# Performance work log

Hardware: AMD Instinct MI355X
Metric: run time of the kernel (lower is better)

The kernel has to match this reference:

```python
import jax, jax.numpy as jnp
import numpy as np

D = 256; H = 8; HD = D // H; L = 6; NQ = 100; DFF = 2048
FREQS = np.geomspace(1.0, 512.0, 10).astype(np.float32)  # WorldSpacePE: 10 freqs up to 512


def _ln(x, g, b, eps=1e-5):
    m = x.mean(-1, keepdims=True)
    v = ((x - m) ** 2).mean(-1, keepdims=True)
    return (x - m) * jax.lax.rsqrt(v + eps) * g + b


def _mha(q, k, v, Wq, bq, Wk, bk, Wv, bv, Wo, bo, bias=None):
    # standard nn.MultiheadAttention math (batch_first, eval mode -> no dropout)
    B, Q, _ = q.shape; N = k.shape[1]
    qh = (q @ Wq + bq).reshape(B, Q, H, HD).transpose(0, 2, 1, 3)
    kh = (k @ Wk + bk).reshape(B, N, H, HD).transpose(0, 2, 1, 3)
    vh = (v @ Wv + bv).reshape(B, N, H, HD).transpose(0, 2, 1, 3)
    s = jnp.einsum('bhqd,bhkd->bhqk', qh, kh) / np.float32(np.sqrt(HD))
    if bias is not None:
        s = s + bias
    a = jax.nn.softmax(s, axis=-1)
    o = jnp.einsum('bhqk,bhkd->bhqd', a, vh).transpose(0, 2, 1, 3).reshape(B, Q, D)
    return o @ Wo + bo


def setup_inputs() -> dict:
    key = jax.random.key(0)
    cnt = [0]
    def nk():
        cnt[0] += 1
        return jax.random.fold_in(key, cnt[0])
    def rn(shape, scale=0.02):
        return (jax.random.normal(nk(), shape) * scale).astype(jnp.float32)
    def zeros(shape):
        return jnp.zeros(shape, jnp.float32)
    def ones(shape):
        return jnp.ones(shape, jnp.float32)
    B, N, NT = 8, 4096, 32
    inp = {
        'image_feats': jax.random.normal(nk(), (B, N, D), jnp.float32),
        'text_feats': jax.random.normal(nk(), (B, NT, 256), jnp.float32),
        'pointmap': jax.random.normal(nk(), (B, N, 3), jnp.float32),
        'query_embed': rn((NQ, D)),
        'presence_tok': rn((1, D)),
        'text_proj_W': rn((256, D)), 'text_proj_b': zeros((D,)),
        'tWq': rn((D, D)), 'tbq': zeros((D,)), 'tWk': rn((D, D)), 'tbk': zeros((D,)),
        'tWv': rn((D, D)), 'tbv': zeros((D,)), 'tWo': rn((D, D)), 'tbo': zeros((D,)),
        'tln_g': ones((D,)), 'tln_b': zeros((D,)),
        'wpe_W': rn((60, D)), 'wpe_b': zeros((D,)),
        'sa_Wq': rn((L, D, D)), 'sa_bq': zeros((L, D)), 'sa_Wk': rn((L, D, D)), 'sa_bk': zeros((L, D)),
        'sa_Wv': rn((L, D, D)), 'sa_bv': zeros((L, D)), 'sa_Wo': rn((L, D, D)), 'sa_bo': zeros((L, D)),
        'ca_Wq': rn((L, D, D)), 'ca_bq': zeros((L, D)), 'ca_Wk': rn((L, D, D)), 'ca_bk': zeros((L, D)),
        'ca_Wv': rn((L, D, D)), 'ca_bv': zeros((L, D)), 'ca_Wo': rn((L, D, D)), 'ca_bo': zeros((L, D)),
        'ffn_W1': rn((L, D, DFF)), 'ffn_b1': zeros((L, DFF)),
        'ffn_W2': rn((L, DFF, D)), 'ffn_b2': zeros((L, D)),
        'ln1_g': ones((L, D)), 'ln1_b': zeros((L, D)),
        'ln2_g': ones((L, D)), 'ln2_b': zeros((L, D)),
        'ln3_g': ones((L, D)), 'ln3_b': zeros((L, D)),
        'pos_W': rn((L, D, 3)), 'pos_b': zeros((L, 3)),
        'beta': ones((L, H)),  # gasa_beta_init = 1.0
        'fin_g': ones((D,)), 'fin_b': zeros((D,)),
        'pW1': rn((D, D)), 'pb1': zeros((D,)),
        'pW2': rn((D, D)), 'pb2': zeros((D,)),
        'pW3': rn((D, 1)), 'pb3': zeros((1,)),
    }
    return inp


def reference(image_feats, text_feats, pointmap, query_embed, presence_tok,
              text_proj_W, text_proj_b,
              tWq, tbq, tWk, tbk, tWv, tbv, tWo, tbo, tln_g, tln_b,
              wpe_W, wpe_b,
              sa_Wq, sa_bq, sa_Wk, sa_bk, sa_Wv, sa_bv, sa_Wo, sa_bo,
              ca_Wq, ca_bq, ca_Wk, ca_bk, ca_Wv, ca_bv, ca_Wo, ca_bo,
              ffn_W1, ffn_b1, ffn_W2, ffn_b2,
              ln1_g, ln1_b, ln2_g, ln2_b, ln3_g, ln3_b,
              pos_W, pos_b, beta, fin_g, fin_b,
              pW1, pb1, pW2, pb2, pW3, pb3):
    B, N, _ = image_feats.shape
    # --- world-space PE from pointmap (sin/cos over 10 freqs, 3 coords -> 60d -> D) ---
    ang = pointmap[..., None] * jnp.asarray(FREQS)            # [B,N,3,10]
    enc = jnp.concatenate([jnp.sin(ang), jnp.cos(ang)], -1).reshape(B, N, 60)
    mem = image_feats + enc @ wpe_W + wpe_b                   # PE added to memory
    # --- text conditioning of queries ---
    txt = text_feats @ text_proj_W + text_proj_b              # [B,NT,D]
    x = jnp.concatenate([
        jnp.broadcast_to(query_embed, (B, NQ, D)),
        jnp.broadcast_to(presence_tok, (B, 1, D)),
    ], axis=1)                                                # [B,101,D]
    x = _ln(x + _mha(x, txt, txt, tWq, tbq, tWk, tbk, tWv, tbv, tWo, tbo), tln_g, tln_b)
    # --- decoder layers with GASA geometric attention bias (post-norm) ---
    for i in range(L):
        x = _ln(x + _mha(x, x, x, sa_Wq[i], sa_bq[i], sa_Wk[i], sa_bk[i],
                         sa_Wv[i], sa_bv[i], sa_Wo[i], sa_bo[i]), ln1_g[i], ln1_b[i])
        pos_q = x @ pos_W[i] + pos_b[i]                       # [B,101,3] predicted 3D pos
        d2 = jnp.sum((pos_q[:, :, None, :] - pointmap[:, None, :, :]) ** 2, -1)  # [B,101,N]
        bias = -jax.nn.softplus(beta[i])[None, :, None, None] * d2[:, None]      # [B,H,101,N]
        x = _ln(x + _mha(x, mem, mem, ca_Wq[i], ca_bq[i], ca_Wk[i], ca_bk[i],
                         ca_Wv[i], ca_bv[i], ca_Wo[i], ca_bo[i], bias=bias), ln2_g[i], ln2_b[i])
        h = jax.nn.relu(x @ ffn_W1[i] + ffn_b1[i]) @ ffn_W2[i] + ffn_b2[i]
        x = _ln(x + h, ln3_g[i], ln3_b[i])
    x = _ln(x, fin_g, fin_b)
    hs = x[:, :NQ]                                            # [B,100,D]
    pres = x[:, NQ]                                           # [B,D]
    h = jax.nn.relu(pres @ pW1 + pb1)
    h = jax.nn.relu(h @ pW2 + pb2)
    presence_logit = h @ pW3 + pb3                            # [B,1]
    return hs, presence_logit
```

## Files before the change

### kernel.cpp

```cpp
#include <hip/hip_runtime.h>
#include <math.h>

#define DD 256
#define NH 8
#define HDIM 32
#define NLAY 6
#define NQRY 100
#define TT 101
#define BB 8
#define NN 4096
#define NTXT 32
#define FFD 2048
#define MM (BB*TT)
#define MMP 896
#define BNN (BB*NN)
#define KC 8
#define KPC (NN/KC)
#define D2 (DD*DD)
#define C1S 0.25506807170842403f

typedef __bf16 bf16x8 __attribute__((ext_vector_type(8)));
typedef float f32x4v __attribute__((ext_vector_type(4)));
typedef unsigned int u32x4 __attribute__((ext_vector_type(4)));
typedef unsigned int u32x2 __attribute__((ext_vector_type(2)));

__device__ __forceinline__ ushort f2b(float f) {
  unsigned u = __builtin_bit_cast(unsigned, f);
  u += 0x7FFF + ((u >> 16) & 1);
  return (ushort)(u >> 16);
}
__device__ __forceinline__ unsigned pk2(float lo, float hi) {
  return (unsigned)f2b(lo) | ((unsigned)f2b(hi) << 16);
}
__device__ __forceinline__ f32x4v mfma16(bf16x8 a, bf16x8 b, f32x4v c) {
  return __builtin_amdgcn_mfma_f32_16x16x32_bf16(a, b, c, 0, 0, 0);
}

__device__ __forceinline__ void gload16(const void* g, void* l) {
  __builtin_amdgcn_global_load_lds(
      (const __attribute__((address_space(1))) void*)g,
      (__attribute__((address_space(3))) void*)l, 16, 0, 0);
}

template <int NROWS>
__device__ __forceinline__ void stage_sw(const ushort* __restrict__ G, size_t ldg,
                                         int row0, int k0, char* lds, int w, int l) {
  constexpr int RPW = NROWS / 4;
  constexpr int ISSUES = RPW / 8;
#pragma unroll
  for (int p = 0; p < ISSUES; ++p) {
    int slot = p * 64 + l;
    int row = w * RPW + (slot >> 3);
    int blk = slot & 7;
    int cb = blk ^ (row & 7);
    const ushort* src = G + (size_t)(row0 + row) * ldg + (size_t)k0 + cb * 8;
    char* db = lds + (w * RPW + p * 8) * 128;
    gload16(src, db);
  }
}

template <int NROWS>
__device__ __forceinline__ void stage2(const ushort* __restrict__ G, size_t ldg,
                                       int row0, int k0, char* lds, int w, int l) {
  constexpr int RPW = NROWS / 4;
  constexpr int ISSUES = RPW / 4;
#pragma unroll
  for (int p = 0; p < ISSUES; ++p) {
    int row = w * RPW + p * 4 + (l >> 4);
    int blk = l & 15;
    int cb = (blk & 8) | ((blk & 7) ^ (row & 7));
    const ushort* src = G + (size_t)(row0 + row) * ldg + (size_t)k0 + cb * 8;
    char* db = lds + (w * RPW + p * 4) * 256;
    gload16(src, db);
  }
}

__device__ __forceinline__ void gemm_core(const ushort* __restrict__ A, size_t lda,
                                          const ushort* __restrict__ Bt, size_t ldb,
                                          int m0, int n0, int kBeg, int kEnd,
                                          char* AsB, char* BsB, int t,
                                          f32x4v acc[2][4]) {
  int w = t >> 6, l = t & 63, lq = l & 15, lg = l >> 4;
  for (int k0 = kBeg; k0 < kEnd; k0 += 64) {
    __syncthreads();
    stage_sw<128>(A, lda, m0, k0, AsB, w, l);
    stage_sw<64>(Bt, ldb, n0, k0, BsB, w, l);
    __syncthreads();
#pragma unroll
    for (int ks = 0; ks < 2; ++ks) {
      bf16x8 af[2], bfr[4];
#pragma unroll
      for (int mt = 0; mt < 2; ++mt) {
        int row = w * 32 + mt * 16 + lq;
        int kb = ks * 64 + lg * 16;
        af[mt] = __builtin_bit_cast(
            bf16x8, *(const u32x4*)(AsB + row * 128 + (kb ^ ((row & 7) << 4))));
      }
#pragma unroll
      for (int nt = 0; nt < 4; ++nt) {
        int row = nt * 16 + lq;
        int kb = ks * 64 + lg * 16;
        bfr[nt] = __builtin_bit_cast(
            bf16x8, *(const u32x4*)(BsB + row * 128 + (kb ^ ((row & 7) << 4))));
      }
#pragma unroll
      for (int mt = 0; mt < 2; ++mt)
#pragma unroll
        for (int nt = 0; nt < 4; ++nt) acc[mt][nt] = mfma16(af[mt], bfr[nt], acc[mt][nt]);
    }
  }
}

__device__ __forceinline__ void gemm_core128(const ushort* __restrict__ A, size_t lda,
                                             const ushort* __restrict__ Bt, size_t ldb,
                                             int m0, int n0, int kBeg, int kEnd,
                                             char* AsB, char* BsB, int t,
                                             f32x4v acc[2][4]) {
  int w = t >> 6, l = t & 63, lq = l & 15, lg = l >> 4;
  for (int k0 = kBeg; k0 < kEnd; k0 += 128) {
    __syncthreads();
    stage2<128>(A, lda, m0, k0, AsB, w, l);
    stage2<64>(Bt, ldb, n0, k0, BsB, w, l);
    __syncthreads();
#pragma unroll
    for (int ks = 0; ks < 4; ++ks) {
      int kb = ks * 64 + lg * 16;
      bf16x8 af[2], bfr[4];
#pragma unroll
      for (int mt = 0; mt < 2; ++mt) {
        int row = w * 32 + mt * 16 + lq;
        af[mt] = __builtin_bit_cast(
            bf16x8, *(const u32x4*)(AsB + row * 256 + (kb ^ ((row & 7) << 4))));
      }
#pragma unroll
      for (int nt = 0; nt < 4; ++nt) {
        int row = nt * 16 + lq;
        bfr[nt] = __builtin_bit_cast(
            bf16x8, *(const u32x4*)(BsB + row * 256 + (kb ^ ((row & 7) << 4))));
      }
#pragma unroll
      for (int mt = 0; mt < 2; ++mt)
#pragma unroll
        for (int nt = 0; nt < 4; ++nt) acc[mt][nt] = mfma16(af[mt], bfr[nt], acc[mt][nt]);
    }
  }
}

__global__ __launch_bounds__(256) void k_enc(const float* __restrict__ pm,
                                             ushort* __restrict__ encb) {
  int t = threadIdx.x;
  int row = blockIdx.x * 32 + (t >> 3);
  int kb = (t & 7) * 8;
  ushort o[8];
#pragma unroll
  for (int u = 0; u < 8; ++u) {
    int k = kb + u;
    float val = 0.f;
    if (k < 60) {
      int c = k / 20, jj = k % 20;
      float f = (float)(1 << (jj % 10));
      float a = pm[(size_t)row * 3 + c] * f;
      val = (jj < 10) ? sinf(a) : cosf(a);
    }
    o[u] = f2b(val);
  }
  *(u32x4*)(encb + (size_t)row * 64 + kb) = *(const u32x4*)o;
}

__global__ __launch_bounds__(256) void k_wpet(const float* __restrict__ wpeW,
                                              ushort* __restrict__ wpeT) {
  int n = blockIdx.x * 16 + (threadIdx.x >> 4);
  int k = (threadIdx.x & 15) * 4;
  ushort o[4];
#pragma unroll
  for (int u = 0; u < 4; ++u) {
    int kk = k + u;
    o[u] = (kk < 60) ? f2b(wpeW[(size_t)kk * DD + n]) : (ushort)0;
  }
  *(u32x2*)(wpeT + (size_t)n * 64 + k) = *(const u32x2*)o;
}

__global__ __launch_bounds__(256) void k_gemm_mem(const ushort* __restrict__ encb,
                                                  const ushort* __restrict__ wpeT,
                                                  const float* __restrict__ wpeb,
                                                  const float* __restrict__ img,
                                                  ushort* __restrict__ memb) {
  __shared__ __align__(16) char AsB[16384];
  __shared__ __align__(16) char BsB[8192];
  int m0 = blockIdx.x * 128, n0 = blockIdx.y * 64;
  f32x4v acc[2][4] = {};
  gemm_core(encb, 64, wpeT, 64, m0, n0, 0, 64, AsB, BsB, threadIdx.x, acc);
  int t = threadIdx.x, w = t >> 6, l = t & 63, lq = l & 15, lg = l >> 4;
#pragma unroll
  for (int nt = 0; nt < 4; ++nt) {
    int n = n0 + nt * 16 + lq;
    float bv = wpeb[n];
#pragma unroll
    for (int mt = 0; mt < 2; ++mt) {
      int rowg = m0 + w * 32 + mt * 16 + lg * 4;
      f32x4v a = acc[mt][nt];
#pragma unroll
      for (int r = 0; r < 4; ++r)
        memb[(size_t)(rowg + r) * DD + n] = f2b(a[r] + bv + img[(size_t)(rowg + r) * DD + n]);
    }
  }
}

struct T2BArgs {
  const float* fam[8];
  const float* single[5];
  const float* fW1; const float* fW2;
  ushort* wT; ushort* w1T; ushort* w2T;
};
__global__ __launch_bounds__(256) void k_t2b_all(T2BArgs a) {
  __shared__ ushort T[64][72];
  int id = blockIdx.x;
  const float* src; ushort* dst; int K, N, k0, n0;
  if (id < 768) {
    int fam = id / 96, rem = id % 96, mi = rem >> 4, ti = rem & 15;
    src = a.fam[fam] + (size_t)mi * D2;
    dst = a.wT + (size_t)(fam * 6 + mi) * D2;
    K = DD; N = DD; k0 = (ti >> 2) * 64; n0 = (ti & 3) * 64;
  } else if (id < 848) {
    int j = (id - 768) >> 4, ti = (id - 768) & 15;
    src = a.single[j];
    dst = a.wT + (size_t)(48 + j) * D2;
    K = DD; N = DD; k0 = (ti >> 2) * 64; n0 = (ti & 3) * 64;
  } else if (id < 1616) {
    int t2 = id - 848, mi = t2 >> 7, ti = t2 & 127;
    src = a.fW1 + (size_t)mi * DD * FFD;
    dst = a.w1T + (size_t)mi * DD * FFD;
    K = DD; N = FFD; k0 = (ti >> 5) * 64; n0 = (ti & 31) * 64;
  } else {
    int t2 = id - 1616, mi = t2 >> 7, ti = t2 & 127;
    src = a.fW2 + (size_t)mi * DD * FFD;
    dst = a.w2T + (size_t)mi * DD * FFD;
    K = FFD; N = DD; k0 = (ti >> 2) * 64; n0 = (ti & 3) * 64;
  }
  int t = threadIdx.x;
  int kk = t >> 4, nn4 = (t & 15) * 4;
#pragma unroll
  for (int p = 0; p < 4; ++p) {
    int krow = kk + p * 16;
    float4 v = *(const float4*)(src + (size_t)(k0 + krow) * N + n0 + nn4);
    T[nn4 + 0][krow] = f2b(v.x);
    T[nn4 + 1][krow] = f2b(v.y);
    T[nn4 + 2][krow] = f2b(v.z);
    T[nn4 + 3][krow] = f2b(v.w);
  }
  __syncthreads();
  int nn = t >> 3, kk8 = (t & 7) * 8;
#pragma unroll
  for (int p = 0; p < 2; ++p) {
    int nrow = nn + p * 32;
    u32x4 v = *(const u32x4*)(&T[nrow][kk8]);
    *(u32x4*)(dst + (size_t)(n0 + nrow) * K + k0 + kk8) = v;
  }
}

__global__ __launch_bounds__(256) void k_pm4(const float* __restrict__ pm,
                                             float4* __restrict__ pm4) {
  int i = blockIdx.x * 256 + threadIdx.x;
  float x = pm[(size_t)i * 3 + 0];
  float y = pm[(size_t)i * 3 + 1];
  float z = pm[(size_t)i * 3 + 2];
  float4 v;
  v.x = x; v.y = y; v.z = z; v.w = x * x + y * y + z * z;
  pm4[i] = v;
}

__global__ __launch_bounds__(256) void k_f2b(const float* __restrict__ in,
                                             ushort* __restrict__ out, int n) {
  int i = (blockIdx.x * 256 + threadIdx.x) * 4;
  if (i + 3 < n) {
    float4 v = *(const float4*)(in + i);
    out[i + 0] = f2b(v.x);
    out[i + 1] = f2b(v.y);
    out[i + 2] = f2b(v.z);
    out[i + 3] = f2b(v.w);
  }
}

template <int OM>
__global__ __launch_bounds__(256) void k_gemm_gen(const ushort* __restrict__ A,
                                                  const ushort* __restrict__ Bt,
                                                  const float* __restrict__ bias,
                                                  void* __restrict__ C, int Nc) {
  __shared__ __align__(16) char AsB[32768];
  __shared__ __align__(16) char BsB[16384];
  int m0 = blockIdx.x * 128, n0 = blockIdx.y * 64;
  f32x4v acc[2][4] = {};
  gemm_core128(A, 256, Bt, 256, m0, n0, 0, 256, AsB, BsB, threadIdx.x, acc);
  int t = threadIdx.x, w = t >> 6, l = t & 63, lq = l & 15, lg = l >> 4;
#pragma unroll
  for (int nt = 0; nt < 4; ++nt) {
    int n = n0 + nt * 16 + lq;
    float bv = bias[n];
#pragma unroll
    for (int mt = 0; mt < 2; ++mt) {
      int rowg = m0 + w * 32 + mt * 16 + lg * 4;
      f32x4v a = acc[mt][nt];
      a[0] += bv; a[1] += bv; a[2] += bv; a[3] += bv;
      if (OM == 2) {
        a[0] = fmaxf(a[0], 0.f); a[1] = fmaxf(a[1], 0.f);
        a[2] = fmaxf(a[2], 0.f); a[3] = fmaxf(a[3], 0.f);
      }
      if (OM == 3) { a[0] *= C1S; a[1] *= C1S; a[2] *= C1S; a[3] *= C1S; }
      if (OM == 0) {
        float* Cf = (float*)C;
#pragma unroll
        for (int r = 0; r < 4; ++r) Cf[(size_t)(rowg + r) * Nc + n] = a[r];
      } else {
        ushort* Cb = (ushort*)C;
#pragma unroll
        for (int r = 0; r < 4; ++r) Cb[(size_t)(rowg + r) * Nc + n] = f2b(a[r]);
      }
    }
  }
}

__global__ __launch_bounds__(256) void k_qkv_kv(
    const ushort* __restrict__ xbA, const ushort* __restrict__ Bq,
    const ushort* __restrict__ Bk, const ushort* __restrict__ Bv,
    const float* __restrict__ bq, const float* __restrict__ bk,
    const float* __restrict__ bv, ushort* __restrict__ Qb,
    ushort* __restrict__ Kbs, ushort* __restrict__ Vst,
    const ushort* __restrict__ memb, const ushort* __restrict__ Btk,
    const ushort* __restrict__ Btv, const float* __restrict__ cbk,
    const float* __restrict__ cbv, ushort* __restrict__ Kb,
    ushort* __restrict__ Vt) {
  __shared__ __align__(16) char LB[65536];
  int bid = blockIdx.x;
  int t = threadIdx.x, w = t >> 6, l = t & 63, lq = l & 15, lg = l >> 4;
  if (bid < 84) {
    char* AsB = LB;
    char* BsB = LB + 32768;
    int m0 = (bid % 7) * 128;
    int yy = bid / 7;
    int sel = yy >> 2;
    int n0 = (yy & 3) * 64;
    const ushort* Bt = sel == 0 ? Bq : (sel == 1 ? Bk : Bv);
    const float* bias = sel == 0 ? bq : (sel == 1 ? bk : bv);
    f32x4v acc[2][4] = {};
    gemm_core128(xbA, 256, Bt, 256, m0, n0, 0, 256, AsB, BsB, t, acc);
#pragma unroll
    for (int nt = 0; nt < 4; ++nt) {
      int n = n0 + nt * 16 + lq;
      float bvv = bias[n];
#pragma unroll
      for (int mt = 0; mt < 2; ++mt) {
        int rowg = m0 + w * 32 + mt * 16 + lg * 4;
        f32x4v a = acc[mt][nt];
        a[0] += bvv; a[1] += bvv; a[2] += bvv; a[3] += bvv;
        if (sel == 0) {
#pragma unroll
          for (int r = 0; r < 4; ++r) Qb[(size_t)(rowg + r) * DD + n] = f2b(a[r] * C1S);
        } else if (sel == 1) {
#pragma unroll
          for (int r = 0; r < 4; ++r) Kbs[(size_t)(rowg + r) * DD + n] = f2b(a[r]);
        } else {
          int h = n >> 5, dd = n & 31;
#pragma unroll
          for (int r = 0; r < 4; ++r) {
            int rg = rowg + r;
            if (rg < MM) {
              int b = rg / TT, tq = rg % TT;
              Vst[((size_t)((b * 8 + h) * 32 + dd)) * 128 + tq] = f2b(a[r]);
            }
          }
        }
      }
    }
  } else {
    char* AsB = LB;
    char* BsB = LB + 32768;
    int tile = bid - 84;
    int m0 = (tile & 255) * 128;
    int yy = tile >> 8;
    int isV = yy >= 2;
    int n0 = (yy & 1) * 128;
    const ushort* Bt = isV ? Btv : Btk;
    f32x4v acc[2][8] = {};
    for (int k0 = 0; k0 < 256; k0 += 128) {
      __syncthreads();
      stage2<128>(memb, 256, m0, k0, AsB, w, l);
      stage2<128>(Bt, 256, n0, k0, BsB, w, l);
      __syncthreads();
#pragma unroll
      for (int ks = 0; ks < 4; ++ks) {
        int kb = ks * 64 + lg * 16;
        bf16x8 af[2], bfr[8];
#pragma unroll
        for (int mt = 0; mt < 2; ++mt) {
          int row = w * 32 + mt * 16 + lq;
          af[mt] = __builtin_bit_cast(
              bf16x8, *(const u32x4*)(AsB + row * 256 + (kb ^ ((row & 7) << 4))));
        }
#pragma unroll
        for (int nt = 0; nt < 8; ++nt) {
          int row = nt * 16 + lq;
          bfr[nt] = __builtin_bit_cast(
              bf16x8, *(const u32x4*)(BsB + row * 256 + (kb ^ ((row & 7) << 4))));
        }
#pragma unroll
        for (int mt = 0; mt < 2; ++mt)
#pragma unroll
          for (int nt = 0; nt < 8; ++nt) acc[mt][nt] = mfma16(af[mt], bfr[nt], acc[mt][nt]);
      }
    }
    if (!isV) {
#pragma unroll
      for (int nt = 0; nt < 8; ++nt) {
        int n = n0 + nt * 16 + lq;
        float bvv = cbk[n];
#pragma unroll
        for (int mt = 0; mt < 2; ++mt) {
          int rowg = m0 + w * 32 + mt * 16 + lg * 4;
          f32x4v a = acc[mt][nt];
#pragma unroll
          for (int r = 0; r < 4; ++r) Kb[(size_t)(rowg + r) * DD + n] = f2b(a[r] + bvv);
        }
      }
    } else {
      ushort* T = (ushort*)LB;
      __syncthreads();
#pragma unroll
      for (int nt = 0; nt < 8; ++nt) {
        int ddl = nt * 16 + lq;
        float bvv = cbv[n0 + ddl];
#pragma unroll
        for (int mt = 0; mt < 2; ++mt) {
          int kl = w * 32 + mt * 16 + lg * 4;
          f32x4v a = acc[mt][nt];
          u32x2 pv;
          pv[0] = pk2(a[0] + bvv, a[1] + bvv);
          pv[1] = pk2(a[2] + bvv, a[3] + bvv);
          *(u32x2*)(T + ddl * 136 + kl) = pv;
        }
      }
      __syncthreads();
      int row = t >> 1, half = t & 1;
      int b = m0 >> 12, key0 = m0 & 4095;
      const ushort* src = T + row * 136 + half * 64;
      ushort* dst = Vt + ((size_t)(b * 256 + n0 + row)) * 4096 + key0 + half * 64;
#pragma unroll
      for (int i = 0; i < 8; ++i)
        *(u32x4*)(dst + i * 8) = *(const u32x4*)(src + i * 8);
    }
  }
}

template <int QPROJ>
__global__ __launch_bounds__(256) void k_gemm_o_ln(
    const ushort* __restrict__ A, const ushort* __restrict__ WoT,
    const float* __restrict__ bo, const float* __restrict__ xres,
    const float* __restrict__ g, const float* __restrict__ be,
    float* __restrict__ xout, ushort* __restrict__ xbout,
    const float* __restrict__ Wp, const float* __restrict__ bp,
    float* __restrict__ pqout) {
  __shared__ __align__(16) char LB[81920];
  char* AsB = LB;
  char* BsB = LB + 16384;
  int m0 = blockIdx.x * 64;
  int t = threadIdx.x, w = t >> 6, l = t & 63, lq = l & 15, lg = l >> 4;
  f32x4v acc[16] = {};
  for (int k0 = 0; k0 < 256; k0 += 128) {
    __syncthreads();
    stage2<64>(A, 256, m0, k0, AsB, w, l);
    stage2<256>(WoT, 256, 0, k0, BsB, w, l);
    __syncthreads();
#pragma unroll
    for (int ks = 0; ks < 4; ++ks) {
      int kb = ks * 64 + lg * 16;
      int arow = w * 16 + lq;
      bf16x8 af = __builtin_bit_cast(
          bf16x8, *(const u32x4*)(AsB + arow * 256 + (kb ^ ((arow & 7) << 4))));
#pragma unroll
      for (int nt = 0; nt < 16; ++nt) {
        int brow = nt * 16 + lq;
        bf16x8 bf = __builtin_bit_cast(
            bf16x8, *(const u32x4*)(BsB + brow * 256 + (kb ^ ((brow & 7) << 4))));
        acc[nt] = mfma16(af, bf, acc[nt]);
      }
    }
  }
  int rowb = m0 + w * 16 + lg * 4;
  float s[4] = {}, s2[4] = {};
#pragma unroll
  for (int nt = 0; nt < 16; ++nt) {
    int col = nt * 16 + lq;
    float bv = bo[col];
    f32x4v a = acc[nt];
#pragma unroll
    for (int r = 0; r < 4; ++r) {
      a[r] += bv + xres[(size_t)(rowb + r) * DD + col];
      s[r] += a[r];
      s2[r] += a[r] * a[r];
    }
    acc[nt] = a;
  }
#pragma unroll
  for (int r = 0; r < 4; ++r) {
#pragma unroll
    for (int o = 1; o < 16; o <<= 1) {
      s[r] += __shfl_xor(s[r], o, 64);
      s2[r] += __shfl_xor(s2[r], o, 64);
    }
  }
  float mu[4], inv[4];
#pragma unroll
  for (int r = 0; r < 4; ++r) {
    mu[r] = s[r] * (1.f / DD);
    float var = s2[r] * (1.f / DD) - mu[r] * mu[r];
    inv[r] = rsqrtf(var + 1e-5f);
  }
  float pp0[4] = {}, pp1[4] = {}, pp2[4] = {};
#pragma unroll
  for (int nt = 0; nt < 16; ++nt) {
    int col = nt * 16 + lq;
    float gd = g[col], bd = be[col];
    float w0 = 0.f, w1 = 0.f, w2 = 0.f;
    if (QPROJ) { w0 = Wp[col * 3]; w1 = Wp[col * 3 + 1]; w2 = Wp[col * 3 + 2]; }
#pragma unroll
    for (int r = 0; r < 4; ++r) {
      float ln = (acc[nt][r] - mu[r]) * inv[r] * gd + bd;
      xout[(size_t)(rowb + r) * DD + col] = ln;
      xbout[(size_t)(rowb + r) * DD + col] = f2b(ln);
      if (QPROJ) { pp0[r] += ln * w0; pp1[r] += ln * w1; pp2[r] += ln * w2; }
    }
  }
  if (QPROJ) {
#pragma unroll
    for (int r = 0; r < 4; ++r) {
#pragma unroll
      for (int o = 1; o < 16; o <<= 1) {
        pp0[r] += __shfl_xor(pp0[r], o, 64);
        pp1[r] += __shfl_xor(pp1[r], o, 64);
        pp2[r] += __shfl_xor(pp2[r], o, 64);
      }
      if (lq == 0) {
        pqout[(size_t)(rowb + r) * 3 + 0] = pp0[r] + bp[0];
        pqout[(size_t)(rowb + r) * 3 + 1] = pp1[r] + bp[1];
        pqout[(size_t)(rowb + r) * 3 + 2] = pp2[r] + bp[2];
      }
    }
  }
}

__global__ __launch_bounds__(256) void k_init_x(const float* __restrict__ qe,
                                                const float* __restrict__ pt,
                                                float* __restrict__ x,
                                                ushort* __restrict__ xb) {
  int r = blockIdx.x, d = threadIdx.x;
  int t = r % TT;
  float v = (t < NQRY) ? qe[t * DD + d] : pt[d];
  x[(size_t)r * DD + d] = v;
  xb[(size_t)r * DD + d] = f2b(v);
}

__global__ __launch_bounds__(128) void k_attn_small(const float* __restrict__ q,
                                                    const float* __restrict__ k,
                                                    const float* __restrict__ v,
                                                    ushort* __restrict__ out,
                                                    int NK) {
  int bh = blockIdx.x;
  int b = bh >> 3, h = bh & 7;
  __shared__ float Ks[TT][HDIM];
  __shared__ float Vs[TT][HDIM];
  for (int i = threadIdx.x; i < NK * HDIM; i += 128) {
    int n = i >> 5, j = i & 31;
    Ks[n][j] = k[(size_t)(b * NK + n) * DD + h * HDIM + j];
    Vs[n][j] = v[(size_t)(b * NK + n) * DD + h * HDIM + j];
  }
  __syncthreads();
  int t = threadIdx.x;
  if (t >= TT) return;
  float qv[HDIM];
  const float* qp = q + (size_t)(b * TT + t) * DD + h * HDIM;
#pragma unroll
  for (int j = 0; j < HDIM; ++j) qv[j] = qp[j];
  const float sc = 0.17677669529663687f * 1.4426950408889634f;
  float l = 0.f, acc[HDIM] = {};
  for (int n = 0; n < NK; ++n) {
    float s = 0.f;
#pragma unroll
    for (int j = 0; j < HDIM; ++j) s += qv[j] * Ks[n][j];
    float p = exp2f(s * sc);
    l += p;
#pragma unroll
    for (int j = 0; j < HDIM; ++j) acc[j] += p * Vs[n][j];
  }
  float inv = 1.f / l;
  ushort* op = out + (size_t)(b * TT + t) * DD + h * HDIM;
#pragma unroll
  for (int j = 0; j < HDIM; ++j) op[j] = f2b(acc[j] * inv);
}

__global__ __launch_bounds__(256) void k_self_mfma(const ushort* __restrict__ Qb,
                                                   const ushort* __restrict__ Kbs,
                                                   const ushort* __restrict__ Vst,
                                                   ushort* __restrict__ out) {
  int bh = blockIdx.x;
  int b = bh >> 3, h = bh & 7;
  int t = threadIdx.x, w = t >> 6, l = t & 63, lq = l & 15, lg = l >> 4;
  __shared__ ushort Plds[4][2][16][40];
  const f32x4v Z = {0.f, 0.f, 0.f, 0.f};
  bf16x8 qfb[2];
  f32x4v oacc[2][2] = {};
  float lsum[2] = {0.f, 0.f};
#pragma unroll
  for (int qi = 0; qi < 2; ++qi) {
    int qidx = (w * 2 + qi) * 16 + lq;
    int qc = qidx < TT ? qidx : TT - 1;
    qfb[qi] = __builtin_bit_cast(
        bf16x8, *(const u32x4*)(Qb + (size_t)(b * TT + qc) * DD + h * HDIM + lg * 8));
  }
  for (int kk = 0; kk < 128; kk += 32) {
    bf16x8 kf[2], vf[2];
#pragma unroll
    for (int t2 = 0; t2 < 2; ++t2) {
      int key = kk + t2 * 16 + lq;
      int kc2 = key < TT ? key : TT - 1;
      kf[t2] = __builtin_bit_cast(
          bf16x8, *(const u32x4*)(Kbs + (size_t)(b * TT + kc2) * DD + h * HDIM + lg * 8));
    }
#pragma unroll
    for (int dt = 0; dt < 2; ++dt)
      vf[dt] = __builtin_bit_cast(
          bf16x8, *(const u32x4*)(Vst + (size_t)(bh * 32 + dt * 16 + lq) * 128 + kk + lg * 8));
#pragma unroll
    for (int qi = 0; qi < 2; ++qi) {
      f32x4v s0 = mfma16(kf[0], qfb[qi], Z);
      f32x4v s1 = mfma16(kf[1], qfb[qi], Z);
      float p[2][4];
#pragma unroll
      for (int t2 = 0; t2 < 2; ++t2) {
#pragma unroll
        for (int r = 0; r < 4; ++r) {
          int kr = kk + t2 * 16 + lg * 4 + r;
          float sv = (t2 == 0) ? s0[r] : s1[r];
          p[t2][r] = (kr < TT) ? exp2f(sv) : 0.f;
        }
        lsum[qi] += (p[t2][0] + p[t2][1]) + (p[t2][2] + p[t2][3]);
      }
      u32x2 w0, w1;
      w0[0] = pk2(p[0][0], p[0][1]);
      w0[1] = pk2(p[0][2], p[0][3]);
      w1[0] = pk2(p[1][0], p[1][1]);
      w1[1] = pk2(p[1][2], p[1][3]);
      *(u32x2*)(&Plds[w][qi][lq][lg * 4]) = w0;
      *(u32x2*)(&Plds[w][qi][lq][16 + lg * 4]) = w1;
      bf16x8 pf = __builtin_bit_cast(bf16x8, *(const u32x4*)(&Plds[w][qi][lq][lg * 8]));
      oacc[qi][0] = mfma16(vf[0], pf, oacc[qi][0]);
      oacc[qi][1] = mfma16(vf[1], pf, oacc[qi][1]);
    }
  }
#pragma unroll
  for (int qi = 0; qi < 2; ++qi) {
    float lv = lsum[qi];
    lv += __shfl_xor(lv, 16, 64);
    lv += __shfl_xor(lv, 32, 64);
    float inv = 1.f / lv;
    int qidx = (w * 2 + qi) * 16 + lq;
    if (qidx < TT) {
      ushort* op = out + (size_t)(b * TT + qidx) * DD + h * HDIM;
#pragma unroll
      for (int dt = 0; dt < 2; ++dt)
#pragma unroll
        for (int r = 0; r < 4; ++r)
          op[dt * 16 + lg * 4 + r] = f2b(oacc[qi][dt][r] * inv);
    }
  }
}

__global__ __launch_bounds__(256) void k_ffn2sk(const ushort* __restrict__ A,
                                                const ushort* __restrict__ Bt,
                                                float* __restrict__ P) {
  __shared__ __align__(16) char AsB[32768];
  __shared__ __align__(16) char BsB[16384];
  int m0 = blockIdx.x * 128, n0 = blockIdx.y * 64, z = blockIdx.z;
  f32x4v acc[2][4] = {};
  gemm_core128(A, FFD, Bt, FFD, m0, n0, z * 256, z * 256 + 256, AsB, BsB, threadIdx.x, acc);
  int t = threadIdx.x, w = t >> 6, l = t & 63, lq = l & 15, lg = l >> 4;
#pragma unroll
  for (int nt = 0; nt < 4; ++nt) {
    int n = n0 + nt * 16 + lq;
#pragma unroll
    for (int mt = 0; mt < 2; ++mt) {
      int rowg = m0 + w * 32 + mt * 16 + lg * 4;
      f32x4v a = acc[mt][nt];
#pragma unroll
      for (int r = 0; r < 4; ++r)
        P[((size_t)z * MMP + rowg + r) * DD + n] = a[r];
    }
  }
}

__global__ __launch_bounds__(256) void k_red_ln3(const float* __restrict__ P,
                                                 const float* __restrict__ bias,
                                                 const float* __restrict__ xres,
                                                 const float* __restrict__ g,
                                                 const float* __restrict__ be,
                                                 float* __restrict__ xout,
                                                 ushort* __restrict__ xbout) {
  int row = blockIdx.x, d = threadIdx.x;
  float a = xres[(size_t)row * DD + d] + bias[d];
#pragma unroll
  for (int z = 0; z < 8; ++z) a += P[((size_t)z * MMP + row) * DD + d];
  float s = a, s2 = a * a;
#pragma unroll
  for (int o = 1; o < 64; o <<= 1) {
    s += __shfl_xor(s, o, 64);
    s2 += __shfl_xor(s2, o, 64);
  }
  __shared__ float ws[4], ws2[4];
  int wid = d >> 6;
  if ((d & 63) == 0) { ws[wid] = s; ws2[wid] = s2; }
  __syncthreads();
  s = ws[0] + ws[1] + ws[2] + ws[3];
  s2 = ws2[0] + ws2[1] + ws2[2] + ws2[3];
  float m = s * (1.f / DD);
  float var = s2 * (1.f / DD) - m * m;
  float inv = rsqrtf(var + 1e-5f);
  float r_ = (a - m) * inv * g[d] + be[d];
  xout[(size_t)row * DD + d] = r_;
  xbout[(size_t)row * DD + d] = f2b(r_);
}

__global__ __launch_bounds__(256) void k_cross_mfma(
    const ushort* __restrict__ Qb, const ushort* __restrict__ Kb,
    const ushort* __restrict__ Vt, const float* __restrict__ posq,
    const float4* __restrict__ pm4, const float* __restrict__ betaL,
    float* __restrict__ pacc, float* __restrict__ pl) {
  int bh = blockIdx.x, kc = blockIdx.y;
  int b = bh >> 3, h = bh & 7;
  int t = threadIdx.x, w = t >> 6, l = t & 63, lq = l & 15, lg = l >> 4;
  const float L2E = 1.4426950408889634f;
  float spb = log1pf(expf(betaL[h]));
  float cb = spb * L2E;

  __shared__ float4 pm4s[KPC];
  __shared__ ushort Plds[4][2][16][40];

  int kbase = b * NN + kc * KPC;
  for (int i = t; i < KPC; i += 256) pm4s[i] = pm4[kbase + i];
  __syncthreads();

  const f32x4v Z = {0.f, 0.f, 0.f, 0.f};
  bf16x8 qfb[2];
  float a0[2], px[2], py[2], pz[2];
  f32x4v oacc[2][2] = {};
  float lsum[2] = {0.f, 0.f};

#pragma unroll
  for (int qi = 0; qi < 2; ++qi) {
    int qt = w * 2 + qi;
    int qidx = qt * 16 + lq;
    int qc = qidx < TT ? qidx : TT - 1;
    size_t xr = (size_t)(b * TT + qc);
    qfb[qi] = __builtin_bit_cast(
        bf16x8, *(const u32x4*)(Qb + xr * 256 + h * 32 + lg * 8));
    float qx = posq[xr * 3 + 0], qy = posq[xr * 3 + 1], qz = posq[xr * 3 + 2];
    a0[qi] = -cb * (qx * qx + qy * qy + qz * qz);
    px[qi] = 2.f * cb * qx;
    py[qi] = 2.f * cb * qy;
    pz[qi] = 2.f * cb * qz;
  }

  for (int kk = 0; kk < KPC; kk += 32) {
    bf16x8 kf[2], vf[2];
#pragma unroll
    for (int t2 = 0; t2 < 2; ++t2)
      kf[t2] = __builtin_bit_cast(
          bf16x8, *(const u32x4*)(Kb + (size_t)(kbase + kk + t2 * 16 + lq) * 256 +
                                  h * 32 + lg * 8));
#pragma unroll
    for (int dt = 0; dt < 2; ++dt)
      vf[dt] = __builtin_bit_cast(
          bf16x8, *(const u32x4*)(Vt + (size_t)(bh * 32 + dt * 16 + lq) * 4096 +
                                  kc * KPC + kk + lg * 8));
    float bx[2][4], by[2][4], bz[2][4], b0[2][4];
#pragma unroll
    for (int t2 = 0; t2 < 2; ++t2)
#pragma unroll
      for (int r = 0; r < 4; ++r) {
        float4 pv = pm4s[kk + t2 * 16 + lg * 4 + r];
        bx[t2][r] = pv.x; by[t2][r] = pv.y; bz[t2][r] = pv.z;
        b0[t2][r] = cb * pv.w;
      }
#pragma unroll
    for (int qi = 0; qi < 2; ++qi) {
      f32x4v s0 = mfma16(kf[0], qfb[qi], Z);
      f32x4v s1 = mfma16(kf[1], qfb[qi], Z);
      float p[2][4];
#pragma unroll
      for (int t2 = 0; t2 < 2; ++t2) {
#pragma unroll
        for (int r = 0; r < 4; ++r) {
          float sv = (t2 == 0) ? s0[r] : s1[r];
          float bias = fmaf(px[qi], bx[t2][r],
                       fmaf(py[qi], by[t2][r],
                       fmaf(pz[qi], bz[t2][r], a0[qi] - b0[t2][r])));
          p[t2][r] = exp2f(sv + bias);
        }
        lsum[qi] += (p[t2][0] + p[t2][1]) + (p[t2][2] + p[t2][3]);
      }
      u32x2 w0, w1;
      w0[0] = pk2(p[0][0], p[0][1]);
      w0[1] = pk2(p[0][2], p[0][3]);
      w1[0] = pk2(p[1][0], p[1][1]);
      w1[1] = pk2(p[1][2], p[1][3]);
      *(u32x2*)(&Plds[w][qi][lq][lg * 4]) = w0;
      *(u32x2*)(&Plds[w][qi][lq][16 + lg * 4]) = w1;
      bf16x8 pf = __builtin_bit_cast(bf16x8, *(const u32x4*)(&Plds[w][qi][lq][lg * 8]));
      oacc[qi][0] = mfma16(vf[0], pf, oacc[qi][0]);
      oacc[qi][1] = mfma16(vf[1], pf, oacc[qi][1]);
    }
  }

#pragma unroll
  for (int qi = 0; qi < 2; ++qi) {
    float lv = lsum[qi];
    lv += __shfl_xor(lv, 16, 64);
    lv += __shfl_xor(lv, 32, 64);
    int qt = w * 2 + qi;
    int qidx = qt * 16 + lq;
    if (qidx < TT) {
      size_t o = ((size_t)(kc * 64 + bh) * TT + qidx) * 32;
#pragma unroll
      for (int dt = 0; dt < 2; ++dt) {
        f32x4v a = oacc[qi][dt];
        float4 st;
        st.x = a[0]; st.y = a[1]; st.z = a[2]; st.w = a[3];
        *(float4*)(pacc + o + dt * 16 + lg * 4) = st;
      }
      if (lg == 0) pl[(size_t)(kc * 64 + bh) * TT + qidx] = lv;
    }
  }
}

__global__ __launch_bounds__(256) void k_cross_merge(const float* __restrict__ pacc,
                                                     const float* __restrict__ pl,
                                                     ushort* __restrict__ out) {
  int bh = blockIdx.x;
  int b = bh >> 3, h = bh & 7;
  int q8 = blockIdx.y * 8 + (threadIdx.x >> 5);
  int j = threadIdx.x & 31;
  if (q8 >= TT) return;
  float sa = 0.f, sl = 0.f;
  for (int kc = 0; kc < KC; ++kc) {
    sa += pacc[(((size_t)kc * 64 + bh) * TT + q8) * HDIM + j];
    sl += pl[((size_t)kc * 64 + bh) * TT + q8];
  }
  out[((size_t)(b * TT + q8)) * DD + h * HDIM + j] = f2b(sa / sl);
}

__global__ __launch_bounds__(256) void k_fin(const float* __restrict__ x,
                                             const float* __restrict__ g,
                                             const float* __restrict__ be,
                                             float* __restrict__ hs,
                                             float* __restrict__ pres) {
  int row = blockIdx.x, d = threadIdx.x;
  int b = row / TT, tq = row % TT;
  float v = x[(size_t)row * DD + d];
  float s = v, s2 = v * v;
#pragma unroll
  for (int o = 1; o < 64; o <<= 1) {
    s += __shfl_xor(s, o, 64);
    s2 += __shfl_xor(s2, o, 64);
  }
  __shared__ float ws[4], ws2[4];
  int wid = d >> 6;
  if ((d & 63) == 0) { ws[wid] = s; ws2[wid] = s2; }
  __syncthreads();
  s = ws[0] + ws[1] + ws[2] + ws[3];
  s2 = ws2[0] + ws2[1] + ws2[2] + ws2[3];
  float m = s * (1.f / DD);
  float var = s2 * (1.f / DD) - m * m;
  float inv = rsqrtf(var + 1e-5f);
  float r = (v - m) * inv * g[d] + be[d];
  if (tq < NQRY) hs[((size_t)(b * NQRY + tq)) * DD + d] = r;
  else pres[(size_t)b * DD + d] = r;
}

__global__ __launch_bounds__(256) void k_mlp8(const float* __restrict__ in,
                                              const float* __restrict__ W,
                                              const float* __restrict__ b,
                                              float* __restrict__ out) {
  __shared__ float ins[8][DD];
  __shared__ float red[8][32][8];
  int t = threadIdx.x;
  for (int i = t; i < 8 * DD; i += 256) ins[i >> 8][i & 255] = in[i];
  __syncthreads();
  int c = t & 31, ks = t >> 5;
  int cg = blockIdx.x * 32 + c;
  float acc[8] = {};
  for (int k = ks * 32; k < ks * 32 + 32; ++k) {
    float w = W[(size_t)k * DD + cg];
#pragma unroll
    for (int r = 0; r < 8; ++r) acc[r] += ins[r][k] * w;
  }
#pragma unroll
  for (int r = 0; r < 8; ++r) red[ks][c][r] = acc[r];
  __syncthreads();
  int c2 = t & 31, r2 = t >> 5;
  float s = 0.f;
#pragma unroll
  for (int k2 = 0; k2 < 8; ++k2) s += red[k2][c2][r2];
  s = fmaxf(s + b[blockIdx.x * 32 + c2], 0.f);
  out[(size_t)r2 * DD + blockIdx.x * 32 + c2] = s;
}

__global__ __launch_bounds__(256) void k_logit(const float* __restrict__ h2,
                                               const float* __restrict__ W3,
                                               const float* __restrict__ b3,
                                               float* __restrict__ out) {
  int r = threadIdx.x >> 5, lane = threadIdx.x & 31;
  float s = 0.f;
  for (int k = lane; k < DD; k += 32) s += h2[r * DD + k] * W3[k];
#pragma unroll
  for (int o = 16; o; o >>= 1) s += __shfl_xor(s, o, 32);
  if (lane == 0) out[r] = s + b3[0];
}

extern "C" void kernel_launch(void* const* d_in, const int* in_sizes, int n_in,
                              void* d_out, int out_size, void* d_ws, size_t ws_size,
                              hipStream_t stream) {
  (void)in_sizes; (void)n_in; (void)out_size; (void)ws_size;
  auto F = [&](int i) { return (const float*)d_in[i]; };
  const float* img   = F(0);
  const float* txtf  = F(1);
  const float* pm    = F(2);
  const float* qe    = F(3);
  const float* ptok  = F(4);
  const float* tpW   = F(5);
  const float* tpb   = F(6);
  const float* tWq   = F(7);  const float* tbq = F(8);
  const float* tWk   = F(9);  const float* tbk = F(10);
  const float* tWv   = F(11); const float* tbv = F(12);
  const float* tWo   = F(13); const float* tbo = F(14);
  const float* tlng  = F(15); const float* tlnb = F(16);
  const float* wpeW  = F(17); const float* wpeb = F(18);
  const float* saWq  = F(19); const float* sabq = F(20);
  const float* saWk  = F(21); const float* sabk = F(22);
  const float* saWv  = F(23); const float* sabv = F(24);
  const float* saWo  = F(25); const float* sabo = F(26);
  const float* caWq  = F(27); const float* cabq = F(28);
  const float* caWk  = F(29); const float* cabk = F(30);
  const float* caWv  = F(31); const float* cabv = F(32);
  const float* caWo  = F(33); const float* cabo = F(34);
  const float* fW1   = F(35); const float* fb1 = F(36);
  const float* fW2   = F(37); const float* fb2 = F(38);
  const float* ln1g  = F(39); const float* ln1b = F(40);
  const float* ln2g  = F(41); const float* ln2b = F(42);
  const float* ln3g  = F(43); const float* ln3b = F(44);
  const float* posW  = F(45); const float* posb = F(46);
  const float* beta  = F(47);
  const float* fing  = F(48); const float* finb = F(49);
  const float* pW1   = F(50); const float* pb1 = F(51);
  const float* pW2   = F(52); const float* pb2 = F(53);
  const float* pW3   = F(54); const float* pb3 = F(55);

  char* wp = (char*)d_ws;
  auto alloc = [&](size_t bytes) {
    char* p = wp;
    wp += (bytes + 255) & ~(size_t)255;
    return (void*)p;
  };
  ushort* memb = (ushort*)alloc((size_t)BNN * DD * 2);
  ushort* Kb   = (ushort*)alloc((size_t)BNN * DD * 2);
  ushort* Vt   = (ushort*)alloc((size_t)64 * 32 * 4096 * 2);
  ushort* encb = (ushort*)alloc((size_t)BNN * 64 * 2);
  ushort* wT   = (ushort*)alloc((size_t)53 * D2 * 2);
  ushort* w1T  = (ushort*)alloc((size_t)6 * FFD * DD * 2);
  ushort* w2T  = (ushort*)alloc((size_t)6 * DD * FFD * 2);
  ushort* xb   = (ushort*)alloc((size_t)MMP * DD * 2);
  ushort* hb   = (ushort*)alloc((size_t)MMP * FFD * 2);
  ushort* tDb  = (ushort*)alloc((size_t)MMP * DD * 2);
  ushort* tQb  = (ushort*)alloc((size_t)MMP * DD * 2);
  ushort* tKb  = (ushort*)alloc((size_t)MMP * DD * 2);
  ushort* tQb2 = (ushort*)alloc((size_t)MMP * DD * 2);
  ushort* Vst  = (ushort*)alloc((size_t)64 * 32 * 128 * 2);
  ushort* txtb = (ushort*)alloc((size_t)BB * NTXT * DD * 2);
  ushort* txtb2= (ushort*)alloc((size_t)BB * NTXT * DD * 2);
  float* fp2  = (float*)alloc((size_t)8 * MMP * DD * 4);
  float* x    = (float*)alloc((size_t)MMP * DD * 4);
  float* tA   = (float*)alloc((size_t)MMP * DD * 4);
  float* tK   = (float*)alloc((size_t)BB * NTXT * DD * 4);
  float* tV   = (float*)alloc((size_t)BB * NTXT * DD * 4);
  float* pacc = (float*)alloc((size_t)(KC * 64 + 8) * TT * HDIM * 4);
  float* pl   = (float*)alloc((size_t)(KC * 64 + 8) * TT * 4);
  float* posq = (float*)alloc((size_t)4096 * 4);
  float4* pm4 = (float4*)alloc((size_t)BNN * 16);
  float* pres = (float*)alloc((size_t)BB * DD * 4);
  float* ph1  = (float*)alloc((size_t)BB * DD * 4);
  float* ph2  = (float*)alloc((size_t)BB * DD * 4);
  ushort* wpeT = (ushort*)alloc((size_t)DD * 64 * 2);

  k_enc<<<BNN / 32, 256, 0, stream>>>(pm, encb);
  k_wpet<<<16, 256, 0, stream>>>(wpeW, wpeT);
  k_pm4<<<BNN / 256, 256, 0, stream>>>(pm, pm4);
  T2BArgs ta;
  ta.fam[0] = saWq; ta.fam[1] = saWk; ta.fam[2] = saWv; ta.fam[3] = saWo;
  ta.fam[4] = caWq; ta.fam[5] = caWk; ta.fam[6] = caWv; ta.fam[7] = caWo;
  ta.single[0] = tpW; ta.single[1] = tWq; ta.single[2] = tWk;
  ta.single[3] = tWv; ta.single[4] = tWo;
  ta.fW1 = fW1; ta.fW2 = fW2; ta.wT = wT; ta.w1T = w1T; ta.w2T = w2T;
  k_t2b_all<<<2384, 256, 0, stream>>>(ta);
  k_gemm_mem<<<dim3(256, 4), 256, 0, stream>>>(encb, wpeT, wpeb, img, memb);

  k_f2b<<<(BB * NTXT * DD) / 1024, 256, 0, stream>>>(txtf, txtb, BB * NTXT * DD);
  k_gemm_gen<1><<<dim3(2, 4), 256, 0, stream>>>(txtb, wT + (size_t)48 * D2, tpb, txtb2, DD);
  k_gemm_gen<0><<<dim3(2, 4), 256, 0, stream>>>(txtb2, wT + (size_t)50 * D2, tbk, tK, DD);
  k_gemm_gen<0><<<dim3(2, 4), 256, 0, stream>>>(txtb2, wT + (size_t)51 * D2, tbv, tV, DD);
  k_init_x<<<MM, 256, 0, stream>>>(qe, ptok, x, xb);
  k_gemm_gen<0><<<dim3(7, 4), 256, 0, stream>>>(xb, wT + (size_t)49 * D2, tbq, tA, DD);
  k_attn_small<<<64, 128, 0, stream>>>(tA, tK, tV, tDb, NTXT);
  k_gemm_o_ln<0><<<14, 256, 0, stream>>>(tDb, wT + (size_t)52 * D2, tbo, x, tlng, tlnb,
                                         x, xb, nullptr, nullptr, nullptr);

  for (int i = 0; i < NLAY; ++i) {
    int iD = i * DD;
    k_qkv_kv<<<1108, 256, 0, stream>>>(
        xb, wT + (size_t)(0 + i) * D2, wT + (size_t)(6 + i) * D2, wT + (size_t)(12 + i) * D2,
        sabq + iD, sabk + iD, sabv + iD, tQb, tKb, Vst,
        memb, wT + (size_t)(30 + i) * D2, wT + (size_t)(36 + i) * D2,
        cabk + iD, cabv + iD, Kb, Vt);
    k_self_mfma<<<64, 256, 0, stream>>>(tQb, tKb, Vst, tDb);
    k_gemm_o_ln<1><<<14, 256, 0, stream>>>(tDb, wT + (size_t)(18 + i) * D2, sabo + iD,
                                           x, ln1g + iD, ln1b + iD, x, xb,
                                           posW + (size_t)i * DD * 3, posb + i * 3, posq);
    k_gemm_gen<3><<<dim3(7, 4), 256, 0, stream>>>(xb, wT + (size_t)(24 + i) * D2,
                                                  cabq + iD, tQb2, DD);
    k_cross_mfma<<<dim3(64, KC), 256, 0, stream>>>(tQb2, Kb, Vt, posq, pm4,
                                                   beta + i * NH, pacc, pl);
    k_cross_merge<<<dim3(64, 13), 256, 0, stream>>>(pacc, pl, tDb);
    k_gemm_o_ln<0><<<14, 256, 0, stream>>>(tDb, wT + (size_t)(42 + i) * D2, cabo + iD,
                                           x, ln2g + iD, ln2b + iD, x, xb,
                                           nullptr, nullptr, nullptr);
    k_gemm_gen<2><<<dim3(7, 32), 256, 0, stream>>>(xb, w1T + (size_t)i * DD * FFD,
                                                   fb1 + i * FFD, hb, FFD);
    k_ffn2sk<<<dim3(7, 4, 8), 256, 0, stream>>>(hb, w2T + (size_t)i * DD * FFD, fp2);
    k_red_ln3<<<MM, 256, 0, stream>>>(fp2, fb2 + iD, x, ln3g + iD, ln3b + iD, x, xb);
  }

  k_fin<<<MM, 256, 0, stream>>>(x, fing, finb, (float*)d_out, pres);
  k_mlp8<<<8, 256, 0, stream>>>(pres, pW1, pb1, ph1);
  k_mlp8<<<8, 256, 0, stream>>>(ph1, pW2, pb2, ph2);
  k_logit<<<1, 256, 0, stream>>>(ph2, pW3, pb3, (float*)d_out + (size_t)BB * NQRY * DD);
}
```

Baseline: 701.7 us.

## Compute cross-attn K and V projections in one tile sharing the memory A-tile

Each cross-attention KV block now stages the memory A tile once and multiplies it against both the K and V weight tiles, keeping two accumulator sets. This halves the grid for that part and removes the duplicated A-tile loads. It also folds three prep kernels into one launch and the two text K/V GEMMs into one dual launch. In exchange LDS use rises to 96KB and register pressure doubles, which lowers occupancy.

```diff
diff --git a/kernel.cpp b/kernel.cpp
--- a/kernel.cpp
+++ b/kernel.cpp
@@ -146,38 +146,49 @@
   }
 }
 
-__global__ __launch_bounds__(256) void k_enc(const float* __restrict__ pm,
-                                             ushort* __restrict__ encb) {
+__global__ __launch_bounds__(256) void k_prep(const float* __restrict__ pm,
+                                              const float* __restrict__ wpeW,
+                                              ushort* __restrict__ encb,
+                                              ushort* __restrict__ wpeT,
+                                              float4* __restrict__ pm4) {
+  int id = blockIdx.x;
   int t = threadIdx.x;
-  int row = blockIdx.x * 32 + (t >> 3);
-  int kb = (t & 7) * 8;
-  ushort o[8];
-#pragma unroll
-  for (int u = 0; u < 8; ++u) {
-    int k = kb + u;
-    float val = 0.f;
-    if (k < 60) {
-      int c = k / 20, jj = k % 20;
-      float f = (float)(1 << (jj % 10));
-      float a = pm[(size_t)row * 3 + c] * f;
-      val = (jj < 10) ? sinf(a) : cosf(a);
-    }
-    o[u] = f2b(val);
-  }
-  *(u32x4*)(encb + (size_t)row * 64 + kb) = *(const u32x4*)o;
-}
-
-__global__ __launch_bounds__(256) void k_wpet(const float* __restrict__ wpeW,
-                                              ushort* __restrict__ wpeT) {
-  int n = blockIdx.x * 16 + (threadIdx.x >> 4);
-  int k = (threadIdx.x & 15) * 4;
-  ushort o[4];
-#pragma unroll
-  for (int u = 0; u < 4; ++u) {
-    int kk = k + u;
-    o[u] = (kk < 60) ? f2b(wpeW[(size_t)kk * DD + n]) : (ushort)0;
-  }
-  *(u32x2*)(wpeT + (size_t)n * 64 + k) = *(const u32x2*)o;
+  if (id < 1024) {
+    int row = id * 32 + (t >> 3);
+    int kb = (t & 7) * 8;
+    ushort o[8];
+#pragma unroll
+    for (int u = 0; u < 8; ++u) {
+      int k = kb + u;
+      float val = 0.f;
+      if (k < 60) {
+        int c = k / 20, jj = k % 20;
+        float f = (float)(1 << (jj % 10));
+        float a = pm[(size_t)row * 3 + c] * f;
+        val = (jj < 10) ? sinf(a) : cosf(a);
+      }
+      o[u] = f2b(val);
+    }
+    *(u32x4*)(encb + (size_t)row * 64 + kb) = *(const u32x4*)o;
+  } else if (id < 1040) {
+    int n = (id - 1024) * 16 + (t >> 4);
+    int k = (t & 15) * 4;
+    ushort o[4];
+#pragma unroll
+    for (int u = 0; u < 4; ++u) {
+      int kk = k + u;
+      o[u] = (kk < 60) ? f2b(wpeW[(size_t)kk * DD + n]) : (ushort)0;
+    }
+    *(u32x2*)(wpeT + (size_t)n * 64 + k) = *(const u32x2*)o;
+  } else {
+    int i = (id - 1040) * 256 + t;
+    float x = pm[(size_t)i * 3 + 0];
+    float y = pm[(size_t)i * 3 + 1];
+    float z = pm[(size_t)i * 3 + 2];
+    float4 v;
+    v.x = x; v.y = y; v.z = z; v.w = x * x + y * y + z * z;
+    pm4[i] = v;
+  }
 }
 
 __global__ __launch_bounds__(256) void k_gemm_mem(const ushort* __restrict__ encb,
@@ -258,17 +269,6 @@
   }
 }
 
-__global__ __launch_bounds__(256) void k_pm4(const float* __restrict__ pm,
-                                             float4* __restrict__ pm4) {
-  int i = blockIdx.x * 256 + threadIdx.x;
-  float x = pm[(size_t)i * 3 + 0];
-  float y = pm[(size_t)i * 3 + 1];
-  float z = pm[(size_t)i * 3 + 2];
-  float4 v;
-  v.x = x; v.y = y; v.z = z; v.w = x * x + y * y + z * z;
-  pm4[i] = v;
-}
-
 __global__ __launch_bounds__(256) void k_f2b(const float* __restrict__ in,
                                              ushort* __restrict__ out, int n) {
   int i = (blockIdx.x * 256 + threadIdx.x) * 4;
@@ -319,6 +319,38 @@
   }
 }
 
+__global__ __launch_bounds__(256) void k_gemm_dual(const ushort* __restrict__ A,
+                                                   const ushort* __restrict__ Bt0,
+                                                   const ushort* __restrict__ Bt1,
+                                                   const float* __restrict__ b0,
+                                                   const float* __restrict__ b1,
+                                                   float* __restrict__ C0,
+                                                   float* __restrict__ C1) {
+  __shared__ __align__(16) char AsB[32768];
+  __shared__ __align__(16) char BsB[16384];
+  int sel = blockIdx.y >> 2;
+  int n0 = (blockIdx.y & 3) * 64;
+  int m0 = blockIdx.x * 128;
+  const ushort* Bt = sel ? Bt1 : Bt0;
+  const float* bias = sel ? b1 : b0;
+  float* C = sel ? C1 : C0;
+  f32x4v acc[2][4] = {};
+  gemm_core128(A, 256, Bt, 256, m0, n0, 0, 256, AsB, BsB, threadIdx.x, acc);
+  int t = threadIdx.x, w = t >> 6, l = t & 63, lq = l & 15, lg = l >> 4;
+#pragma unroll
+  for (int nt = 0; nt < 4; ++nt) {
+    int n = n0 + nt * 16 + lq;
+    float bv = bias[n];
+#pragma unroll
+    for (int mt = 0; mt < 2; ++mt) {
+      int rowg = m0 + w * 32 + mt * 16 + lg * 4;
+      f32x4v a = acc[mt][nt];
+#pragma unroll
+      for (int r = 0; r < 4; ++r) C[(size_t)(rowg + r) * DD + n] = a[r] + bv;
+    }
+  }
+}
+
 __global__ __launch_bounds__(256) void k_qkv_kv(
     const ushort* __restrict__ xbA, const ushort* __restrict__ Bq,
     const ushort* __restrict__ Bk, const ushort* __restrict__ Bv,
@@ -329,7 +361,7 @@
     const ushort* __restrict__ Btv, const float* __restrict__ cbk,
     const float* __restrict__ cbv, ushort* __restrict__ Kb,
     ushort* __restrict__ Vt) {
-  __shared__ __align__(16) char LB[65536];
+  __shared__ __align__(16) char LB[98304];
   int bid = blockIdx.x;
   int t = threadIdx.x, w = t >> 6, l = t & 63, lq = l & 15, lg = l >> 4;
   if (bid < 84) {
@@ -373,18 +405,17 @@
     }
   } else {
     char* AsB = LB;
-    char* BsB = LB + 32768;
+    char* BsK = LB + 32768;
+    char* BsV = LB + 65536;
     int tile = bid - 84;
     int m0 = (tile & 255) * 128;
-    int yy = tile >> 8;
-    int isV = yy >= 2;
-    int n0 = (yy & 1) * 128;
-    const ushort* Bt = isV ? Btv : Btk;
-    f32x4v acc[2][8] = {};
+    int n0 = (tile >> 8) * 128;
+    f32x4v accK[2][8] = {}, accV[2][8] = {};
     for (int k0 = 0; k0 < 256; k0 += 128) {
       __syncthreads();
       stage2<128>(memb, 256, m0, k0, AsB, w, l);
-      stage2<128>(Bt, 256, n0, k0, BsB, w, l);
+      stage2<128>(Btk, 256, n0, k0, BsK, w, l);
+      stage2<128>(Btv, 256, n0, k0, BsV, w, l);
       __syncthreads();
 #pragma unroll
       for (int ks = 0; ks < 4; ++ks) {
@@ -400,53 +431,60 @@
         for (int nt = 0; nt < 8; ++nt) {
           int row = nt * 16 + lq;
           bfr[nt] = __builtin_bit_cast(
-              bf16x8, *(const u32x4*)(BsB + row * 256 + (kb ^ ((row & 7) << 4))));
+              bf16x8, *(const u32x4*)(BsK + row * 256 + (kb ^ ((row & 7) << 4))));
         }
 #pragma unroll
         for (int mt = 0; mt < 2; ++mt)
 #pragma unroll
-          for (int nt = 0; nt < 8; ++nt) acc[mt][nt] = mfma16(af[mt], bfr[nt], acc[mt][nt]);
-      }
-    }
-    if (!isV) {
-#pragma unroll
-      for (int nt = 0; nt < 8; ++nt) {
-        int n = n0 + nt * 16 + lq;
-        float bvv = cbk[n];
-#pragma unroll
-        for (int mt = 0; mt < 2; ++mt) {
-          int rowg = m0 + w * 32 + mt * 16 + lg * 4;
-          f32x4v a = acc[mt][nt];
-#pragma unroll
-          for (int r = 0; r < 4; ++r) Kb[(size_t)(rowg + r) * DD + n] = f2b(a[r] + bvv);
+          for (int nt = 0; nt < 8; ++nt) accK[mt][nt] = mfma16(af[mt], bfr[nt], accK[mt][nt]);
+#pragma unroll
+        for (int nt = 0; nt < 8; ++nt) {
+          int row = nt * 16 + lq;
+          bfr[nt] = __builtin_bit_cast(
+              bf16x8, *(const u32x4*)(BsV + row * 256 + (kb ^ ((row & 7) << 4))));
         }
-      }
-    } else {
-      ushort* T = (ushort*)LB;
-      __syncthreads();
-#pragma unroll
-      for (int nt = 0; nt < 8; ++nt) {
-        int ddl = nt * 16 + lq;
-        float bvv = cbv[n0 + ddl];
-#pragma unroll
-        for (int mt = 0; mt < 2; ++mt) {
-          int kl = w * 32 + mt * 16 + lg * 4;
-          f32x4v a = acc[mt][nt];
-          u32x2 pv;
-          pv[0] = pk2(a[0] + bvv, a[1] + bvv);
-          pv[1] = pk2(a[2] + bvv, a[3] + bvv);
-          *(u32x2*)(T + ddl * 136 + kl) = pv;
-        }
-      }
-      __syncthreads();
-      int row = t >> 1, half = t & 1;
-      int b = m0 >> 12, key0 = m0 & 4095;
-      const ushort* src = T + row * 136 + half * 64;
-      ushort* dst = Vt + ((size_t)(b * 256 + n0 + row)) * 4096 + key0 + half * 64;
-#pragma unroll
-      for (int i = 0; i < 8; ++i)
-        *(u32x4*)(dst + i * 8) = *(const u32x4*)(src + i * 8);
-    }
+#pragma unroll
+        for (int mt = 0; mt < 2; ++mt)
+#pragma unroll
+          for (int nt = 0; nt < 8; ++nt) accV[mt][nt] = mfma16(af[mt], bfr[nt], accV[mt][nt]);
+      }
+    }
+#pragma unroll
+    for (int nt = 0; nt < 8; ++nt) {
+      int n = n0 + nt * 16 + lq;
+      float bvv = cbk[n];
+#pragma unroll
+      for (int mt = 0; mt < 2; ++mt) {
+        int rowg = m0 + w * 32 + mt * 16 + lg * 4;
+        f32x4v a = accK[mt][nt];
+#pragma unroll
+        for (int r = 0; r < 4; ++r) Kb[(size_t)(rowg + r) * DD + n] = f2b(a[r] + bvv);
+      }
+    }
+    ushort* T = (ushort*)LB;
+    __syncthreads();
+#pragma unroll
+    for (int nt = 0; nt < 8; ++nt) {
+      int ddl = nt * 16 + lq;
+      float bvv = cbv[n0 + ddl];
+#pragma unroll
+      for (int mt = 0; mt < 2; ++mt) {
+        int kl = w * 32 + mt * 16 + lg * 4;
+        f32x4v a = accV[mt][nt];
+        u32x2 pv;
+        pv[0] = pk2(a[0] + bvv, a[1] + bvv);
+        pv[1] = pk2(a[2] + bvv, a[3] + bvv);
+        *(u32x2*)(T + ddl * 136 + kl) = pv;
+      }
+    }
+    __syncthreads();
+    int row = t >> 1, half = t & 1;
+    int b = m0 >> 12, key0 = m0 & 4095;
+    const ushort* src = T + row * 136 + half * 64;
+    ushort* dst = Vt + ((size_t)(b * 256 + n0 + row)) * 4096 + key0 + half * 64;
+#pragma unroll
+    for (int i = 0; i < 8; ++i)
+      *(u32x4*)(dst + i * 8) = *(const u32x4*)(src + i * 8);
   }
 }
 
@@ -997,9 +1035,7 @@
   float* ph2  = (float*)alloc((size_t)BB * DD * 4);
   ushort* wpeT = (ushort*)alloc((size_t)DD * 64 * 2);
 
-  k_enc<<<BNN / 32, 256, 0, stream>>>(pm, encb);
-  k_wpet<<<16, 256, 0, stream>>>(wpeW, wpeT);
-  k_pm4<<<BNN / 256, 256, 0, stream>>>(pm, pm4);
+  k_prep<<<1168, 256, 0, stream>>>(pm, wpeW, encb, wpeT, pm4);
   T2BArgs ta;
   ta.fam[0] = saWq; ta.fam[1] = saWk; ta.fam[2] = saWv; ta.fam[3] = saWo;
   ta.fam[4] = caWq; ta.fam[5] = caWk; ta.fam[6] = caWv; ta.fam[7] = caWo;
@@ -1011,8 +1047,8 @@
 
   k_f2b<<<(BB * NTXT * DD) / 1024, 256, 0, stream>>>(txtf, txtb, BB * NTXT * DD);
   k_gemm_gen<1><<<dim3(2, 4), 256, 0, stream>>>(txtb, wT + (size_t)48 * D2, tpb, txtb2, DD);
-  k_gemm_gen<0><<<dim3(2, 4), 256, 0, stream>>>(txtb2, wT + (size_t)50 * D2, tbk, tK, DD);
-  k_gemm_gen<0><<<dim3(2, 4), 256, 0, stream>>>(txtb2, wT + (size_t)51 * D2, tbv, tV, DD);
+  k_gemm_dual<<<dim3(2, 8), 256, 0, stream>>>(txtb2, wT + (size_t)50 * D2,
+                                              wT + (size_t)51 * D2, tbk, tbv, tK, tV);
   k_init_x<<<MM, 256, 0, stream>>>(qe, ptok, x, xb);
   k_gemm_gen<0><<<dim3(7, 4), 256, 0, stream>>>(xb, wT + (size_t)49 * D2, tbq, tA, DD);
   k_attn_small<<<64, 128, 0, stream>>>(tA, tK, tV, tDb, NTXT);
@@ -1021,7 +1057,7 @@
 
   for (int i = 0; i < NLAY; ++i) {
     int iD = i * DD;
-    k_qkv_kv<<<1108, 256, 0, stream>>>(
+    k_qkv_kv<<<596, 256, 0, stream>>>(
         xb, wT + (size_t)(0 + i) * D2, wT + (size_t)(6 + i) * D2, wT + (size_t)(12 + i) * D2,
         sabq + iD, sabk + iD, sabv + iD, tQb, tKb, Vst,
         memb, wT + (size_t)(30 + i) * D2, wT + (size_t)(36 + i) * D2,
```

After: 723.2 us. 3.1% more time.
